# Kernel tuning notes

Hardware: AMD Instinct MI355X
Metric: run time of the kernel (lower is better)

The kernel has to match this reference:

```python
import jax, jax.numpy as jnp
import numpy as np

EMBED, HEADS, WIN, UP = 180, 6, 16, 4
HDIM = EMBED // HEADS

def _win_part(x, ws):
    # x: [B, H, W, C] -> [B*(H//ws)*(W//ws), ws, ws, C]
    B, H, W, C = x.shape
    x = x.reshape(B, H // ws, ws, W // ws, ws, C).transpose(0, 1, 3, 2, 4, 5)
    return x.reshape(-1, ws, ws, C)

def _win_rev(w, ws, H, W):
    # inverse of _win_part
    C = w.shape[-1]
    B = w.shape[0] // ((H // ws) * (W // ws))
    x = w.reshape(B, H // ws, W // ws, ws, ws, C).transpose(0, 1, 3, 2, 4, 5)
    return x.reshape(B, H, W, C)

def _ln(x, g, b):
    mu = x.mean(-1, keepdims=True)
    v = ((x - mu) ** 2).mean(-1, keepdims=True)
    return (x - mu) * jax.lax.rsqrt(v + 1e-5) * g + b

def _forward(gumbel_u, x, sel1_w, sel1_b, sel2_w, sel2_b, sel3_w, sel3_b,
             embed_w, embed_b, ln1_g, ln1_b, qkv_w, qkv_b, proj_w, proj_b,
             ln2_g, ln2_b, mlp1_w, mlp1_b, mlp2_w, mlp2_b, up_w, up_b):
    B, C, H, W = x.shape
    ws = H // 4                                     # 64 -> 16 tiles per image
    tiles = _win_part(x.transpose(0, 2, 3, 1), ws)  # [T, ws, ws, C]
    T = tiles.shape[0]
    # --- TileSelection (pooled MLP router) ---
    pooled = tiles.reshape(T, 8, ws // 8, 8, ws // 8, C).mean((2, 4)).reshape(T, 8 * 8 * C)
    f1 = pooled @ sel1_w + sel1_b
    f2 = jax.nn.relu(f1) @ sel2_w + sel2_b
    f3 = jax.nn.relu(f2) @ sel3_w + sel3_b          # [T, 2] routing logits
    # --- hard gumbel-softmax with straight-through estimator (tau=1) ---
    g = -jnp.log(-jnp.log(gumbel_u + 1e-10) + 1e-10)
    y_soft = jax.nn.softmax(f3 + g, axis=-1)
    y_hard = jax.nn.one_hot(jnp.argmax(y_soft, -1), 2, dtype=y_soft.dtype)
    pi = jax.lax.stop_gradient(y_hard - y_soft) + y_soft
    mask = pi[:, 1]                                 # 1 -> transformer expert
    # --- TR expert (SwinIR-style block, dense dispatch over all tiles) ---
    tok = tiles.reshape(T, ws * ws, C) @ embed_w + embed_b   # [T, 4096, 180]
    h = _ln(tok, ln1_g, ln1_b)
    hw = _win_part(h.reshape(T, ws, ws, EMBED), WIN).reshape(-1, WIN * WIN, EMBED)
    Nw, L = hw.shape[0], WIN * WIN
    qkv = (hw @ qkv_w + qkv_b).reshape(Nw, L, 3, HEADS, HDIM)
    q, k, v = qkv[:, :, 0], qkv[:, :, 1], qkv[:, :, 2]
    attn = jax.nn.softmax(jnp.einsum('nlhd,nmhd->nhlm', q, k) / np.sqrt(HDIM).astype(np.float32), axis=-1)
    av = jnp.einsum('nhlm,nmhd->nlhd', attn, v).reshape(Nw, L, EMBED)
    av = av @ proj_w + proj_b
    av = _win_rev(av.reshape(Nw, WIN, WIN, EMBED), WIN, ws, ws).reshape(T, ws * ws, EMBED)
    tok = tok + av
    h2 = _ln(tok, ln2_g, ln2_b)
    tok = tok + jax.nn.gelu(h2 @ mlp1_w + mlp1_b) @ mlp2_w + mlp2_b
    # pixelshuffle x4 upsample: 180 -> 3*4*4
    up = (tok @ up_w + up_b).reshape(T, ws, ws, UP, UP, C)
    up = up.transpose(0, 1, 3, 2, 4, 5).reshape(T, ws * UP, ws * UP, C)
    # --- cheap expert: bicubic x4 ---
    neg = jax.image.resize(tiles, (T, ws * UP, ws * UP, C), method='bicubic')
    # --- combine per-tile and reassemble ---
    m = mask[:, None, None, None]
    sr_tiles = m * up + (1.0 - m) * neg             # [T, 4ws, 4ws, C]
    sr = _win_rev(sr_tiles, H, H * UP, W * UP)      # [B, 4H, 4W, C]
    return sr.transpose(0, 3, 1, 2), f3, f2, f1

def setup_inputs() -> dict:
    key = jax.random.key(0)
    ks = jax.random.split(key, 16)
    B, C, H, W = 1, 3, 256, 256
    T = B * 16
    p = lambda k, s: jax.random.normal(k, s, jnp.float32) * 0.02
    return {
        'x': jax.random.normal(ks[0], (B, C, H, W), jnp.float32),
        'gumbel_u': jax.random.uniform(ks[1], (T, 2), jnp.float32),
        'sel1_w': p(ks[2], (192, 64)), 'sel1_b': jnp.zeros((64,), jnp.float32),
        'sel2_w': p(ks[3], (64, 32)), 'sel2_b': jnp.zeros((32,), jnp.float32),
        'sel3_w': p(ks[4], (32, 2)), 'sel3_b': jnp.zeros((2,), jnp.float32),
        'embed_w': p(ks[5], (3, EMBED)), 'embed_b': jnp.zeros((EMBED,), jnp.float32),
        'ln1_g': jnp.ones((EMBED,), jnp.float32), 'ln1_b': jnp.zeros((EMBED,), jnp.float32),
        'qkv_w': p(ks[6], (EMBED, 3 * EMBED)), 'qkv_b': jnp.zeros((3 * EMBED,), jnp.float32),
        'proj_w': p(ks[7], (EMBED, EMBED)), 'proj_b': jnp.zeros((EMBED,), jnp.float32),
        'ln2_g': jnp.ones((EMBED,), jnp.float32), 'ln2_b': jnp.zeros((EMBED,), jnp.float32),
        'mlp1_w': p(ks[8], (EMBED, 2 * EMBED)), 'mlp1_b': jnp.zeros((2 * EMBED,), jnp.float32),
        'mlp2_w': p(ks[9], (2 * EMBED, EMBED)), 'mlp2_b': jnp.zeros((EMBED,), jnp.float32),
        'up_w': p(ks[10], (EMBED, 3 * UP * UP)), 'up_b': jnp.zeros((3 * UP * UP,), jnp.float32),
    }

def reference(x, gumbel_u, sel1_w, sel1_b, sel2_w, sel2_b, sel3_w, sel3_b,
              embed_w, embed_b, ln1_g, ln1_b, qkv_w, qkv_b, proj_w, proj_b,
              ln2_g, ln2_b, mlp1_w, mlp1_b, mlp2_w, mlp2_b, up_w, up_b):
    return _forward(gumbel_u, x, sel1_w, sel1_b, sel2_w, sel2_b, sel3_w, sel3_b,
                    embed_w, embed_b, ln1_g, ln1_b, qkv_w, qkv_b, proj_w, proj_b,
                    ln2_g, ln2_b, mlp1_w, mlp1_b, mlp2_w, mlp2_b, up_w, up_b)
```

## Files before the change

### kernel.cpp

```cpp
#include <hip/hip_runtime.h>
#include <hip/hip_bf16.h>
#include <cstdint>

typedef __hip_bfloat16 bf16;
typedef __attribute__((ext_vector_type(8))) short short8;
typedef __attribute__((ext_vector_type(4))) short short4v;
typedef __attribute__((ext_vector_type(4))) float f32x4;
typedef __attribute__((ext_vector_type(2))) unsigned int uint2v;

__device__ __forceinline__ float bf2f(bf16 v) { return __bfloat162float(v); }
__device__ __forceinline__ bf16  f2bf(float v) { return __float2bfloat16(v); }
__device__ __forceinline__ float rbf(short s) {
  union { uint32_t u; float f; } c; c.u = ((uint32_t)(uint16_t)s) << 16; return c.f;
}
__device__ __forceinline__ short wbf(float f) {
  bf16 h = f2bf(f); return *(short*)&h;
}
__device__ __forceinline__ uint32_t pack2(float a, float b) {
  bf16 x = f2bf(a), y = f2bf(b);
  return (uint32_t)(*(uint16_t*)&x) | ((uint32_t)(*(uint16_t*)&y) << 16);
}
__device__ __forceinline__ uint2v pack4(float a, float b, float c, float d) {
  uint2v r; r[0] = pack2(a, b); r[1] = pack2(c, d); return r;
}
__device__ __forceinline__ int swz(int row, int g) { return g ^ (row & 7); }

__device__ __forceinline__ int win_to_token(int m) {
  int n = m >> 8, l = m & 255;
  int t = n >> 4, win = n & 15;
  int wi = win >> 2, wj = win & 3;
  int u = l >> 4, v = l & 15;
  return (t << 12) | ((wi * 16 + u) << 6) | (wj * 16 + v);
}

__global__ __launch_bounds__(256) void k_packsel(
    const float* __restrict__ qkvw, const float* __restrict__ projw,
    const float* __restrict__ mlp1w, const float* __restrict__ mlp2w,
    const float* __restrict__ upw, const float* __restrict__ qkvb,
    bf16* __restrict__ Bt_qkv, bf16* __restrict__ Bt_proj,
    bf16* __restrict__ Bt_mlp1, bf16* __restrict__ Bt_mlp2,
    bf16* __restrict__ Bt_up, float* __restrict__ biasq,
    const float* __restrict__ x, const float* __restrict__ gu,
    const float* __restrict__ s1w, const float* __restrict__ s1b,
    const float* __restrict__ s2w, const float* __restrict__ s2b,
    const float* __restrict__ s3w, const float* __restrict__ s3b,
    float* __restrict__ f1o, float* __restrict__ f2o, float* __restrict__ f3o,
    float* __restrict__ maskp) {
  if (blockIdx.x < 1203) {
    int idx = blockIdx.x * 256 + threadIdx.x;
    const int e0 = 576 * 192, e1 = e0 + 192 * 192, e2 = e1 + 384 * 192,
              e3 = e2 + 192 * 384, e4 = e3 + 64 * 192, e5 = e4 + 576;
    if (idx < e0) {
      int np = idx / 192, k = idx % 192;
      int buf = np / 192, colp = np % 192;
      int hd = colp >> 5, dd = colp & 31;
      float v = 0.f;
      if (dd < 30 && k < 180) v = qkvw[(size_t)k * 540 + buf * 180 + hd * 30 + dd];
      Bt_qkv[idx] = f2bf(v);
    } else if (idx < e1) {
      int off = idx - e0; int n = off / 192, kp = off % 192;
      int hd = kp >> 5, dd = kp & 31;
      float v = (dd < 30 && n < 180) ? projw[(size_t)(hd * 30 + dd) * 180 + n] : 0.f;
      Bt_proj[off] = f2bf(v);
    } else if (idx < e2) {
      int off = idx - e1; int n = off / 192, k = off % 192;
      Bt_mlp1[off] = f2bf((k < 180 && n < 360) ? mlp1w[(size_t)k * 360 + n] : 0.f);
    } else if (idx < e3) {
      int off = idx - e2; int n = off / 384, k = off % 384;
      Bt_mlp2[off] = f2bf((k < 360 && n < 180) ? mlp2w[(size_t)k * 180 + n] : 0.f);
    } else if (idx < e4) {
      int off = idx - e3; int n = off / 192, k = off % 192;
      Bt_up[off] = f2bf((k < 180 && n < 48) ? upw[(size_t)k * 48 + n] : 0.f);
    } else if (idx < e5) {
      int np = idx - e4;
      int buf = np / 192, colp = np % 192;
      int hd = colp >> 5, dd = colp & 31;
      biasq[np] = (dd < 30) ? qkvb[buf * 180 + hd * 30 + dd] : 0.f;
    }
    return;
  }
  int t = blockIdx.x - 1203;
  int tid = threadIdx.x;
  int th = t >> 2, tw = t & 3;
  __shared__ float pooled[192];
  __shared__ float red[256];
  __shared__ float f1s[64], f2s[32], f3s[2];
  if (tid < 192) {
    int ch = tid % 3, j = (tid / 3) & 7, i = tid / 24;
    const float* xp = x + ch * 65536 + (th * 64 + i * 8) * 256 + (tw * 64 + j * 8);
    float s = 0.f;
#pragma unroll
    for (int a = 0; a < 8; ++a)
#pragma unroll
      for (int b = 0; b < 8; ++b) s += xp[a * 256 + b];
    pooled[tid] = s * (1.0f / 64.0f);
  }
  __syncthreads();
  {
    int o = tid & 63, part = tid >> 6;
    float s = 0.f;
    for (int k = part * 48; k < part * 48 + 48; ++k) s = fmaf(pooled[k], s1w[k * 64 + o], s);
    red[tid] = s;
  }
  __syncthreads();
  if (tid < 64) {
    float v = red[tid] + red[tid + 64] + red[tid + 128] + red[tid + 192] + s1b[tid];
    f1o[t * 64 + tid] = v;
    f1s[tid] = fmaxf(v, 0.f);
  }
  __syncthreads();
  {
    int o = tid & 31, part = tid >> 5;
    float s = 0.f;
    for (int k = part * 8; k < part * 8 + 8; ++k) s = fmaf(f1s[k], s2w[k * 32 + o], s);
    red[tid] = s;
  }
  __syncthreads();
  if (tid < 32) {
    float v = s2b[tid];
#pragma unroll
    for (int p = 0; p < 8; ++p) v += red[tid + p * 32];
    f2o[t * 32 + tid] = v;
    f2s[tid] = fmaxf(v, 0.f);
  }
  __syncthreads();
  if (tid < 2) {
    float s = s3b[tid];
    for (int k = 0; k < 32; ++k) s = fmaf(f2s[k], s3w[k * 2 + tid], s);
    f3o[t * 2 + tid] = s;
    f3s[tid] = s;
  }
  __syncthreads();
  if (tid == 0) {
    float g0 = -logf(-logf(gu[t * 2 + 0] + 1e-10f) + 1e-10f);
    float g1 = -logf(-logf(gu[t * 2 + 1] + 1e-10f) + 1e-10f);
    maskp[t] = (f3s[1] + g1 > f3s[0] + g0) ? 1.0f : 0.0f;
  }
}

__global__ __launch_bounds__(256) void k_embed(
    const float* __restrict__ x, const float* __restrict__ ew,
    const float* __restrict__ eb, const float* __restrict__ g1,
    const float* __restrict__ b1, bf16* __restrict__ tok,
    bf16* __restrict__ Aq) {
  int wrow = blockIdx.x * 4 + (threadIdx.x >> 6);
  int lane = threadIdx.x & 63;
  int token = win_to_token(wrow);
  int t = token >> 12, p = token & 4095;
  int r = p >> 6, c = p & 63;
  int gh = (t >> 2) * 64 + r, gw = (t & 3) * 64 + c;
  float x0 = x[gh * 256 + gw];
  float x1 = x[65536 + gh * 256 + gw];
  float x2 = x[131072 + gh * 256 + gw];
  float v[3];
  float s = 0.f, s2 = 0.f;
#pragma unroll
  for (int i = 0; i < 3; ++i) {
    int e = lane + i * 64;
    float vv = 0.f;
    if (e < 180) {
      vv = eb[e];
      vv = fmaf(x0, ew[e], vv);
      vv = fmaf(x1, ew[180 + e], vv);
      vv = fmaf(x2, ew[360 + e], vv);
      tok[(size_t)wrow * 180 + e] = f2bf(vv);
      s += vv; s2 = fmaf(vv, vv, s2);
    }
    v[i] = vv;
  }
#pragma unroll
  for (int off = 32; off; off >>= 1) { s += __shfl_xor(s, off); s2 += __shfl_xor(s2, off); }
  float mu = s * (1.f / 180.f);
  float rs = rsqrtf(s2 * (1.f / 180.f) - mu * mu + 1e-5f);
#pragma unroll
  for (int i = 0; i < 3; ++i) {
    int e = lane + i * 64;
    if (e < 192) {
      float a = (e < 180) ? ((v[i] - mu) * rs * g1[e] + b1[e]) : 0.f;
      Aq[(size_t)wrow * 192 + e] = f2bf(a);
    }
  }
}

__global__ __launch_bounds__(512, 2) void k_qkv3(
    const bf16* __restrict__ A, const bf16* __restrict__ Bt,
    const float* __restrict__ biasq, bf16* __restrict__ Qp,
    bf16* __restrict__ Kp, bf16* __restrict__ Vp) {
  __shared__ bf16 Bs[2][64 * 192];
  const int tid = threadIdx.x;
  const int w = tid >> 6, l = tid & 63;
  const int lr = l & 15, lk = l >> 4;
  const int row = blockIdx.x * 128 + w * 16 + lr;

  short8 fa[6];
  {
    const bf16* Ab = A + (size_t)row * 192 + lk * 8;
#pragma unroll
    for (int ks = 0; ks < 6; ++ks) fa[ks] = *(const short8*)(Ab + ks * 32);
  }

  for (int c = tid; c < 1536; c += 512) {
    int n = c / 24, g = c % 24;
    *(short8*)&Bs[0][n * 192 + swz(n, g) * 8] = *(const short8*)(Bt + (size_t)n * 192 + g * 8);
  }

  for (int nt = 0; nt < 9; ++nt) {
    __syncthreads();
    if (nt < 8) {
      const bf16* src = Bt + (size_t)(nt + 1) * 64 * 192;
      bf16* dstb = Bs[(nt + 1) & 1];
      for (int c = tid; c < 1536; c += 512) {
        int n = c / 24, g = c % 24;
        *(short8*)&dstb[n * 192 + swz(n, g) * 8] = *(const short8*)(src + (size_t)n * 192 + g * 8);
      }
    }
    const bf16* Bb = Bs[nt & 1];
    f32x4 acc[4];
#pragma unroll
    for (int j = 0; j < 4; ++j) acc[j] = (f32x4){0.f, 0.f, 0.f, 0.f};
#pragma unroll
    for (int ks = 0; ks < 6; ++ks) {
      short8 fb[4];
#pragma unroll
      for (int j = 0; j < 4; ++j) {
        int rn = j * 16 + lr;
        fb[j] = *(const short8*)&Bb[rn * 192 + swz(rn, ks * 4 + lk) * 8];
      }
#pragma unroll
      for (int j = 0; j < 4; ++j)
        acc[j] = __builtin_amdgcn_mfma_f32_16x16x32_bf16(fb[j], fa[ks], acc[j], 0, 0, 0);
    }
    bf16* dst = (nt < 3) ? Qp : (nt < 6) ? Kp : Vp;
    int c0 = (nt % 3) * 64;
#pragma unroll
    for (int j = 0; j < 4; ++j) {
      int np = nt * 64 + j * 16 + lk * 4;
      f32x4 bv = *(const f32x4*)&biasq[np];
      *(uint2v*)(dst + (size_t)row * 192 + c0 + j * 16 + lk * 4) =
          pack4(acc[j][0] + bv[0], acc[j][1] + bv[1], acc[j][2] + bv[2], acc[j][3] + bv[3]);
    }
  }
}

__global__ __launch_bounds__(256) void k_attn2(
    const bf16* __restrict__ Qp, const bf16* __restrict__ Kp,
    const bf16* __restrict__ Vp, bf16* __restrict__ av) {
  const int blk = blockIdx.x;
  const int win = blk / 6, hd = blk % 6;
  const int tid = threadIdx.x;
  const int w = tid >> 6, l = tid & 63;
  const int lr = l & 15, lk = l >> 4;
  const float scale = 0.18257418583505536f;

  __shared__ bf16 Ks[256][40];
  __shared__ bf16 Vs[32][264];
  __shared__ bf16 Ps[4][16][264];

  {
    const bf16* src = Kp + (size_t)(win * 256 + tid) * 192 + hd * 32;
#pragma unroll
    for (int c = 0; c < 4; ++c)
      *(short8*)&Ks[tid][c * 8] = *(const short8*)(src + c * 8);
  }
  {
    const bf16* src = Vp + (size_t)(win * 256 + tid) * 192 + hd * 32;
    short8 vv[4];
#pragma unroll
    for (int c = 0; c < 4; ++c) vv[c] = *(const short8*)(src + c * 8);
#pragma unroll
    for (int c = 0; c < 4; ++c)
#pragma unroll
      for (int e = 0; e < 8; ++e)
        *(short*)&Vs[c * 8 + e][tid] = vv[c][e];
  }
  __syncthreads();

  for (int qt = 0; qt < 4; ++qt) {
    const int qbase = qt * 64 + w * 16;
    short8 fq = *(const short8*)(Qp + (size_t)(win * 256 + qbase + lr) * 192 + hd * 32 + lk * 8);
    f32x4 accS[16];
#pragma unroll
    for (int kt = 0; kt < 16; ++kt) {
      short8 fk = *(const short8*)(&Ks[kt * 16 + lr][lk * 8]);
      accS[kt] = __builtin_amdgcn_mfma_f32_16x16x32_bf16(
          fk, fq, (f32x4){0.f, 0.f, 0.f, 0.f}, 0, 0, 0);
    }
    float mraw = -1e30f;
#pragma unroll
    for (int kt = 0; kt < 16; ++kt)
#pragma unroll
      for (int r = 0; r < 4; ++r) mraw = fmaxf(mraw, accS[kt][r]);
    mraw = fmaxf(mraw, __shfl_xor(mraw, 16));
    mraw = fmaxf(mraw, __shfl_xor(mraw, 32));
    const float mc = mraw * scale;
    float lsum = 0.f;
#pragma unroll
    for (int kt = 0; kt < 16; ++kt) {
      float p0 = __expf(fmaf(accS[kt][0], scale, -mc));
      float p1 = __expf(fmaf(accS[kt][1], scale, -mc));
      float p2 = __expf(fmaf(accS[kt][2], scale, -mc));
      float p3 = __expf(fmaf(accS[kt][3], scale, -mc));
      lsum += (p0 + p1) + (p2 + p3);
      *(uint32_t*)&Ps[w][lr][kt * 16 + lk * 4]     = pack2(p0, p1);
      *(uint32_t*)&Ps[w][lr][kt * 16 + lk * 4 + 2] = pack2(p2, p3);
    }
    lsum += __shfl_xor(lsum, 16);
    lsum += __shfl_xor(lsum, 32);
    __syncthreads();
    f32x4 accO0 = (f32x4){0.f, 0.f, 0.f, 0.f};
    f32x4 accO1 = (f32x4){0.f, 0.f, 0.f, 0.f};
#pragma unroll
    for (int ks = 0; ks < 8; ++ks) {
      short8 fp  = *(const short8*)(&Ps[w][lr][ks * 32 + lk * 8]);
      short8 fv0 = *(const short8*)(&Vs[lr][ks * 32 + lk * 8]);
      short8 fv1 = *(const short8*)(&Vs[16 + lr][ks * 32 + lk * 8]);
      accO0 = __builtin_amdgcn_mfma_f32_16x16x32_bf16(fv0, fp, accO0, 0, 0, 0);
      accO1 = __builtin_amdgcn_mfma_f32_16x16x32_bf16(fv1, fp, accO1, 0, 0, 0);
    }
    float invl = 1.f / lsum;
    bf16* avrow = av + (size_t)(win * 256 + qbase + lr) * 192 + hd * 32;
    *(uint2v*)(avrow + lk * 4) =
        pack4(accO0[0] * invl, accO0[1] * invl, accO0[2] * invl, accO0[3] * invl);
    *(uint2v*)(avrow + 16 + lk * 4) =
        pack4(accO1[0] * invl, accO1[1] * invl, accO1[2] * invl, accO1[3] * invl);
    __syncthreads();
  }
}

__global__ __launch_bounds__(512, 2) void k_post(
    const bf16* __restrict__ av, const bf16* __restrict__ tok,
    const bf16* __restrict__ Btp, const float* __restrict__ pb,
    const float* __restrict__ g2, const float* __restrict__ b2,
    const bf16* __restrict__ Bt1, const float* __restrict__ b1m,
    const bf16* __restrict__ Bt2, const float* __restrict__ b2m,
    const bf16* __restrict__ Btu, const float* __restrict__ bu,
    bf16* __restrict__ up) {
  __shared__ bf16 Bs[2][64 * 192];
  __shared__ bf16 Hm[128 * 192];
  const int tid = threadIdx.x;
  const int w = tid >> 6, l = tid & 63;
  const int lr = l & 15, lk = l >> 4;
  const int row_l = w * 16 + lr;
  const int row_g = blockIdx.x * 128 + row_l;
  const int half = (lk & 1) * 4;

#define STAGE_A(srcp, dstb)                                               \
  {                                                                       \
    const bf16* _s = (srcp);                                              \
    bf16* _d = (dstb);                                                    \
    for (int c = tid; c < 1536; c += 512) {                               \
      int n = c / 24, g = c % 24;                                         \
      *(short8*)&_d[n * 192 + swz(n, g) * 8] =                            \
          *(const short8*)(_s + (size_t)n * 192 + g * 8);                 \
    }                                                                     \
  }
#define STAGE_S(ntv, dstb)                                                \
  {                                                                       \
    bf16* _d = (dstb);                                                    \
    for (int c = tid; c < 1536; c += 512) {                               \
      int n = c / 8, g = c % 8;                                           \
      *(short8*)&_d[n * 64 + swz(n, g) * 8] =                             \
          *(const short8*)(Bt2 + (size_t)n * 384 + (ntv) * 64 + g * 8);   \
    }                                                                     \
  }

  short8 fa[6];
  {
    const bf16* ab = av + (size_t)row_g * 192 + lk * 8;
#pragma unroll
    for (int ks = 0; ks < 6; ++ks) fa[ks] = *(const short8*)(ab + ks * 32);
  }

  short4v t2p[3][4];
  float sA = 0.f, s2A = 0.f;

  STAGE_A(Btp, Bs[0]);

#pragma unroll
  for (int nt = 0; nt < 3; ++nt) {
    __syncthreads();
    if (nt < 2) { STAGE_A(Btp + (size_t)(nt + 1) * 64 * 192, Bs[(nt + 1) & 1]); }
    else        { STAGE_A(Bt1, Bs[1]); }
    const bf16* Bb = Bs[nt & 1];
    f32x4 acc[4];
#pragma unroll
    for (int j = 0; j < 4; ++j) acc[j] = (f32x4){0.f, 0.f, 0.f, 0.f};
#pragma unroll
    for (int ks = 0; ks < 6; ++ks) {
      short8 fb[4];
#pragma unroll
      for (int j = 0; j < 4; ++j) {
        int rn = j * 16 + lr;
        fb[j] = *(const short8*)&Bb[rn * 192 + swz(rn, ks * 4 + lk) * 8];
      }
#pragma unroll
      for (int j = 0; j < 4; ++j)
        acc[j] = __builtin_amdgcn_mfma_f32_16x16x32_bf16(fb[j], fa[ks], acc[j], 0, 0, 0);
    }
#pragma unroll
    for (int j = 0; j < 4; ++j) {
      int n = nt * 64 + j * 16 + lk * 4;
      if (n < 180) {
        f32x4 bv = *(const f32x4*)&pb[n];
        short4v tv = *(const short4v*)(tok + (size_t)row_g * 180 + n);
#pragma unroll
        for (int q = 0; q < 4; ++q) {
          float v = acc[j][q] + bv[q] + rbf(tv[q]);
          sA += v; s2A = fmaf(v, v, s2A);
          t2p[nt][j][q] = wbf(v);
        }
      } else {
#pragma unroll
        for (int q = 0; q < 4; ++q) t2p[nt][j][q] = 0;
      }
    }
  }

  {
    sA += __shfl_xor(sA, 16);  sA += __shfl_xor(sA, 32);
    s2A += __shfl_xor(s2A, 16); s2A += __shfl_xor(s2A, 32);
    float mu = sA * (1.f / 180.f);
    float rs = rsqrtf(s2A * (1.f / 180.f) - mu * mu + 1e-5f);
#pragma unroll
    for (int nt = 0; nt < 3; ++nt)
#pragma unroll
      for (int j = 0; j < 4; ++j) {
        int n = nt * 64 + j * 16 + lk * 4;
        float h[4] = {0.f, 0.f, 0.f, 0.f};
        if (n < 180) {
          f32x4 gv = *(const f32x4*)&g2[n];
          f32x4 bv = *(const f32x4*)&b2[n];
#pragma unroll
          for (int q = 0; q < 4; ++q)
            h[q] = (rbf(t2p[nt][j][q]) - mu) * rs * gv[q] + bv[q];
        }
        int g = nt * 8 + j * 2 + (lk >> 1);
        *(uint2v*)&Hm[row_l * 192 + swz(row_l, g) * 8 + half] = pack4(h[0], h[1], h[2], h[3]);
      }
  }

  short8 fh[6];
  f32x4 acc2[3][4];
#pragma unroll
  for (int t = 0; t < 3; ++t)
#pragma unroll
    for (int j = 0; j < 4; ++j) acc2[t][j] = (f32x4){0.f, 0.f, 0.f, 0.f};

#pragma unroll
  for (int nt = 0; nt < 6; ++nt) {
    __syncthreads();
    STAGE_S(nt, Bs[0]);
    if (nt == 0) {
#pragma unroll
      for (int ks = 0; ks < 6; ++ks)
        fh[ks] = *(const short8*)&Hm[row_l * 192 + swz(row_l, ks * 4 + lk) * 8];
    }
    {
      const bf16* Bb = Bs[1];
      f32x4 acc1[4];
#pragma unroll
      for (int j = 0; j < 4; ++j) acc1[j] = (f32x4){0.f, 0.f, 0.f, 0.f};
#pragma unroll
      for (int ks = 0; ks < 6; ++ks) {
        short8 fb[4];
#pragma unroll
        for (int j = 0; j < 4; ++j) {
          int rn = j * 16 + lr;
          fb[j] = *(const short8*)&Bb[rn * 192 + swz(rn, ks * 4 + lk) * 8];
        }
#pragma unroll
        for (int j = 0; j < 4; ++j)
          acc1[j] = __builtin_amdgcn_mfma_f32_16x16x32_bf16(fb[j], fh[ks], acc1[j], 0, 0, 0);
      }
#pragma unroll
      for (int j = 0; j < 4; ++j) {
        int n = nt * 64 + j * 16 + lk * 4;
        float m4[4] = {0.f, 0.f, 0.f, 0.f};
        if (n < 360) {
          f32x4 bv = *(const f32x4*)&b1m[n];
#pragma unroll
          for (int q = 0; q < 4; ++q) {
            float v = acc1[j][q] + bv[q];
            float u = 0.7978845608028654f * (v + 0.044715f * v * v * v);
            m4[q] = v / (1.f + __expf(-2.f * u));
          }
        }
        int g = j * 2 + (lk >> 1);
        *(uint2v*)&Hm[row_l * 192 + swz(row_l, g) * 8 + half] = pack4(m4[0], m4[1], m4[2], m4[3]);
      }
    }
    __syncthreads();
    if (nt < 5) { STAGE_A(Bt1 + (size_t)(nt + 1) * 64 * 192, Bs[1]); }
    else        { STAGE_A(Btu, Bs[1]); }
    {
      short8 fm[2];
#pragma unroll
      for (int s = 0; s < 2; ++s)
        fm[s] = *(const short8*)&Hm[row_l * 192 + swz(row_l, s * 4 + lk) * 8];
#pragma unroll
      for (int s = 0; s < 2; ++s)
#pragma unroll
        for (int t = 0; t < 3; ++t)
#pragma unroll
          for (int j = 0; j < 4; ++j) {
            int rn = t * 64 + j * 16 + lr;
            short8 fb2 = *(const short8*)&Bs[0][rn * 64 + swz(rn, s * 4 + lk) * 8];
            acc2[t][j] = __builtin_amdgcn_mfma_f32_16x16x32_bf16(fb2, fm[s], acc2[t][j], 0, 0, 0);
          }
    }
  }

  __syncthreads();
#pragma unroll
  for (int t = 0; t < 3; ++t)
#pragma unroll
    for (int j = 0; j < 4; ++j) {
      int n = t * 64 + j * 16 + lk * 4;
      float o4[4] = {0.f, 0.f, 0.f, 0.f};
      if (n < 180) {
        f32x4 bv = *(const f32x4*)&b2m[n];
#pragma unroll
        for (int q = 0; q < 4; ++q) o4[q] = acc2[t][j][q] + bv[q] + rbf(t2p[t][j][q]);
      }
      int g = t * 8 + j * 2 + (lk >> 1);
      *(uint2v*)&Hm[row_l * 192 + swz(row_l, g) * 8 + half] = pack4(o4[0], o4[1], o4[2], o4[3]);
    }
  __syncthreads();

  short8 ft[6];
#pragma unroll
  for (int ks = 0; ks < 6; ++ks)
    ft[ks] = *(const short8*)&Hm[row_l * 192 + swz(row_l, ks * 4 + lk) * 8];
  f32x4 acc3[3];
#pragma unroll
  for (int j = 0; j < 3; ++j) acc3[j] = (f32x4){0.f, 0.f, 0.f, 0.f};
#pragma unroll
  for (int ks = 0; ks < 6; ++ks) {
    short8 fb[3];
#pragma unroll
    for (int j = 0; j < 3; ++j) {
      int rn = j * 16 + lr;
      fb[j] = *(const short8*)&Bs[1][rn * 192 + swz(rn, ks * 4 + lk) * 8];
    }
#pragma unroll
    for (int j = 0; j < 3; ++j)
      acc3[j] = __builtin_amdgcn_mfma_f32_16x16x32_bf16(fb[j], ft[ks], acc3[j], 0, 0, 0);
  }
#pragma unroll
  for (int j = 0; j < 3; ++j) {
    int n = j * 16 + lk * 4;
    f32x4 bv = *(const f32x4*)&bu[n];
    *(uint2v*)(up + (size_t)row_g * 48 + n) =
        pack4(acc3[j][0] + bv[0], acc3[j][1] + bv[1], acc3[j][2] + bv[2], acc3[j][3] + bv[3]);
  }
#undef STAGE_A
#undef STAGE_S
}

__device__ const float c_cubw[4][4] = {
    {-0.0439453125f, 0.3896484375f, 0.7275390625f, -0.0732421875f},
    {-0.0068359375f, 0.0908203125f, 0.9638671875f, -0.0478515625f},
    {-0.0478515625f, 0.9638671875f, 0.0908203125f, -0.0068359375f},
    {-0.0732421875f, 0.7275390625f, 0.3896484375f, -0.0439453125f},
};

__device__ __forceinline__ void cubw(int r, int ph, float* w, int& base) {
  base = r + ((ph < 2) ? -2 : -1);
  float sum = 0.f;
#pragma unroll
  for (int i = 0; i < 4; ++i) {
    int idx = base + i;
    float wi = (idx >= 0 && idx < 64) ? c_cubw[ph][i] : 0.f;
    w[i] = wi; sum += wi;
  }
  float inv = 1.f / sum;
#pragma unroll
  for (int i = 0; i < 4; ++i) w[i] *= inv;
}

__global__ __launch_bounds__(256) void k_blend(
    const bf16* __restrict__ up, const float* __restrict__ x,
    const float* __restrict__ maskp, float* __restrict__ sr) {
  int idx = blockIdx.x * 256 + threadIdx.x;
  int ch = idx >> 20;
  int rem = idx & 1048575;
  int gR = rem >> 10, gC = rem & 1023;
  int th = gR >> 8, tw = gC >> 8;
  int t = th * 4 + tw;
  int R = gR & 255, C = gC & 255;
  int r = R >> 2, a = R & 3, c = C >> 2, b = C & 3;
  float m = maskp[t];
  float outv;
  if (m > 0.5f) {
    int wi = r >> 4, u = r & 15, wj = c >> 4, v = c & 15;
    int wrow = (t * 16 + wi * 4 + wj) * 256 + u * 16 + v;
    outv = bf2f(up[(size_t)wrow * 48 + a * 12 + b * 3 + ch]);
  } else {
    float wy[4], wx[4];
    int yb, xb;
    cubw(r, a, wy, yb);
    cubw(c, b, wx, xb);
    const float* xc = x + ch * 65536;
    float neg = 0.f;
#pragma unroll
    for (int i = 0; i < 4; ++i) {
      int yi = yb + i;
      if (yi < 0 || yi > 63) continue;
      float rowsum = 0.f;
#pragma unroll
      for (int j = 0; j < 4; ++j) {
        int xj = xb + j;
        if (xj < 0 || xj > 63) continue;
        rowsum = fmaf(wx[j], xc[(th * 64 + yi) * 256 + tw * 64 + xj], rowsum);
      }
      neg = fmaf(wy[i], rowsum, neg);
    }
    outv = neg;
  }
  sr[idx] = outv;
}

extern "C" void kernel_launch(void* const* d_in, const int* in_sizes, int n_in,
                              void* d_out, int out_size, void* d_ws, size_t ws_size,
                              hipStream_t stream) {
  const float* x     = (const float*)d_in[0];
  const float* gu    = (const float*)d_in[1];
  const float* s1w   = (const float*)d_in[2];
  const float* s1b   = (const float*)d_in[3];
  const float* s2w   = (const float*)d_in[4];
  const float* s2b   = (const float*)d_in[5];
  const float* s3w   = (const float*)d_in[6];
  const float* s3b   = (const float*)d_in[7];
  const float* ew    = (const float*)d_in[8];
  const float* ebias = (const float*)d_in[9];
  const float* ln1g  = (const float*)d_in[10];
  const float* ln1b  = (const float*)d_in[11];
  const float* qkvw  = (const float*)d_in[12];
  const float* qkvb  = (const float*)d_in[13];
  const float* projw = (const float*)d_in[14];
  const float* projb = (const float*)d_in[15];
  const float* ln2g  = (const float*)d_in[16];
  const float* ln2b  = (const float*)d_in[17];
  const float* mlp1w = (const float*)d_in[18];
  const float* mlp1b = (const float*)d_in[19];
  const float* mlp2w = (const float*)d_in[20];
  const float* mlp2b = (const float*)d_in[21];
  const float* upw   = (const float*)d_in[22];
  const float* upb   = (const float*)d_in[23];

  float* out = (float*)d_out;
  float* sr  = out;
  float* f3o = out + 3145728;
  float* f2o = f3o + 32;
  float* f1o = f2o + 512;

  char* ws = (char*)d_ws;
  bf16* tok  = (bf16*)(ws);
  bf16* ABuf = (bf16*)(ws + 23592960);
  bf16* Qp   = (bf16*)(ws + 48758784);
  bf16* Kp   = (bf16*)(ws + 73924608);
  bf16* Vp   = (bf16*)(ws + 99090432);
  float* maskp   = (float*)(ws + 124256256);
  bf16* Bt_qkv  = (bf16*)(ws + 124256320);
  bf16* Bt_proj = (bf16*)(ws + 124477504);
  bf16* Bt_mlp1 = (bf16*)(ws + 124551232);
  bf16* Bt_mlp2 = (bf16*)(ws + 124698688);
  bf16* Bt_up   = (bf16*)(ws + 124846144);
  float* biasq  = (float*)(ws + 124870720);
  bf16* up      = (bf16*)(ws + 124873088);
  bf16* av = ABuf;

  k_packsel<<<1219, 256, 0, stream>>>(qkvw, projw, mlp1w, mlp2w, upw, qkvb,
                                      Bt_qkv, Bt_proj, Bt_mlp1, Bt_mlp2, Bt_up, biasq,
                                      x, gu, s1w, s1b, s2w, s2b, s3w, s3b,
                                      f1o, f2o, f3o, maskp);
  k_embed<<<16384, 256, 0, stream>>>(x, ew, ebias, ln1g, ln1b, tok, ABuf);
  k_qkv3<<<512, 512, 0, stream>>>(ABuf, Bt_qkv, biasq, Qp, Kp, Vp);
  k_attn2<<<1536, 256, 0, stream>>>(Qp, Kp, Vp, av);
  k_post<<<512, 512, 0, stream>>>(av, tok, Bt_proj, projb, ln2g, ln2b,
                                  Bt_mlp1, mlp1b, Bt_mlp2, mlp2b, Bt_up, upb, up);
  k_blend<<<12288, 256, 0, stream>>>(up, x, maskp, sr);
}
```

Before: 203.9 us.

## Replace LDS round-trip with cross-lane shuffles in k_post and shrink shared buffer

The k_post kernel no longer writes the LayerNorm output and the MLP residual output to a 128x192 LDS tile and reads them back as MFMA B-fragments. It packs them in registers and rebuilds the operand layout with __shfl gathers, so the staging tile shrinks to a 128x64 buffer used only for the MLP hidden chunk. Less LDS per block, plus launch bounds raised from 2 to 4 blocks per CU, are meant to raise occupancy and drop a barrier. The cost is more shuffle instructions and tighter register limits, which may cause spills.

```diff
diff --git a/kernel.cpp b/kernel.cpp
--- a/kernel.cpp
+++ b/kernel.cpp
@@ -327,7 +327,7 @@
   }
 }
 
-__global__ __launch_bounds__(512, 2) void k_post(
+__global__ __launch_bounds__(512, 4) void k_post(
     const bf16* __restrict__ av, const bf16* __restrict__ tok,
     const bf16* __restrict__ Btp, const float* __restrict__ pb,
     const float* __restrict__ g2, const float* __restrict__ b2,
@@ -336,13 +336,16 @@
     const bf16* __restrict__ Btu, const float* __restrict__ bu,
     bf16* __restrict__ up) {
   __shared__ bf16 Bs[2][64 * 192];
-  __shared__ bf16 Hm[128 * 192];
+  __shared__ bf16 Hmid[128 * 64];
   const int tid = threadIdx.x;
   const int w = tid >> 6, l = tid & 63;
   const int lr = l & 15, lk = l >> 4;
   const int row_l = w * 16 + lr;
   const int row_g = blockIdx.x * 128 + row_l;
   const int half = (lk & 1) * 4;
+  const int sa = lr + 32 * (lk & 1);
+  const int sb = sa + 16;
+  const bool hi2 = (lk >= 2);
 
 #define STAGE_A(srcp, dstb)                                               \
   {                                                                       \
@@ -363,6 +366,24 @@
           *(const short8*)(Bt2 + (size_t)n * 384 + (ntv) * 64 + g * 8);   \
     }                                                                     \
   }
+#define GATHER_FH(dstf, pk, ksv)                                          \
+  {                                                                       \
+    const int _nt = (ksv) >> 1, _jA = ((ksv) & 1) * 2, _jB = _jA + 1;     \
+    uint32_t _a0 = (uint32_t)__shfl((int)pk[_nt][_jA][0], sa);            \
+    uint32_t _a1 = (uint32_t)__shfl((int)pk[_nt][_jA][1], sa);            \
+    uint32_t _b0 = (uint32_t)__shfl((int)pk[_nt][_jB][0], sa);            \
+    uint32_t _b1 = (uint32_t)__shfl((int)pk[_nt][_jB][1], sa);            \
+    uint32_t _c0 = (uint32_t)__shfl((int)pk[_nt][_jA][0], sb);            \
+    uint32_t _c1 = (uint32_t)__shfl((int)pk[_nt][_jA][1], sb);            \
+    uint32_t _d0 = (uint32_t)__shfl((int)pk[_nt][_jB][0], sb);            \
+    uint32_t _d1 = (uint32_t)__shfl((int)pk[_nt][_jB][1], sb);            \
+    uint32_t _t[4];                                                       \
+    _t[0] = hi2 ? _b0 : _a0;                                              \
+    _t[1] = hi2 ? _b1 : _a1;                                              \
+    _t[2] = hi2 ? _d0 : _c0;                                              \
+    _t[3] = hi2 ? _d1 : _c1;                                              \
+    __builtin_memcpy(&(dstf), _t, 16);                                    \
+  }
 
   short8 fa[6];
   {
@@ -416,11 +437,13 @@
     }
   }
 
+  short8 fh[6];
   {
     sA += __shfl_xor(sA, 16);  sA += __shfl_xor(sA, 32);
     s2A += __shfl_xor(s2A, 16); s2A += __shfl_xor(s2A, 32);
     float mu = sA * (1.f / 180.f);
     float rs = rsqrtf(s2A * (1.f / 180.f) - mu * mu + 1e-5f);
+    uint2v hpk[3][4];
 #pragma unroll
     for (int nt = 0; nt < 3; ++nt)
 #pragma unroll
@@ -434,12 +457,12 @@
           for (int q = 0; q < 4; ++q)
             h[q] = (rbf(t2p[nt][j][q]) - mu) * rs * gv[q] + bv[q];
         }
-        int g = nt * 8 + j * 2 + (lk >> 1);
-        *(uint2v*)&Hm[row_l * 192 + swz(row_l, g) * 8 + half] = pack4(h[0], h[1], h[2], h[3]);
-      }
-  }
-
-  short8 fh[6];
+        hpk[nt][j] = pack4(h[0], h[1], h[2], h[3]);
+      }
+#pragma unroll
+    for (int ks = 0; ks < 6; ++ks) GATHER_FH(fh[ks], hpk, ks);
+  }
+
   f32x4 acc2[3][4];
 #pragma unroll
   for (int t = 0; t < 3; ++t)
@@ -450,11 +473,6 @@
   for (int nt = 0; nt < 6; ++nt) {
     __syncthreads();
     STAGE_S(nt, Bs[0]);
-    if (nt == 0) {
-#pragma unroll
-      for (int ks = 0; ks < 6; ++ks)
-        fh[ks] = *(const short8*)&Hm[row_l * 192 + swz(row_l, ks * 4 + lk) * 8];
-    }
     {
       const bf16* Bb = Bs[1];
       f32x4 acc1[4];
@@ -486,7 +504,7 @@
           }
         }
         int g = j * 2 + (lk >> 1);
-        *(uint2v*)&Hm[row_l * 192 + swz(row_l, g) * 8 + half] = pack4(m4[0], m4[1], m4[2], m4[3]);
+        *(uint2v*)&Hmid[row_l * 64 + swz(row_l, g) * 8 + half] = pack4(m4[0], m4[1], m4[2], m4[3]);
       }
     }
     __syncthreads();
@@ -496,7 +514,7 @@
       short8 fm[2];
 #pragma unroll
       for (int s = 0; s < 2; ++s)
-        fm[s] = *(const short8*)&Hm[row_l * 192 + swz(row_l, s * 4 + lk) * 8];
+        fm[s] = *(const short8*)&Hmid[row_l * 64 + swz(row_l, s * 4 + lk) * 8];
 #pragma unroll
       for (int s = 0; s < 2; ++s)
 #pragma unroll
@@ -511,26 +529,26 @@
   }
 
   __syncthreads();
-#pragma unroll
-  for (int t = 0; t < 3; ++t)
-#pragma unroll
-    for (int j = 0; j < 4; ++j) {
-      int n = t * 64 + j * 16 + lk * 4;
-      float o4[4] = {0.f, 0.f, 0.f, 0.f};
-      if (n < 180) {
-        f32x4 bv = *(const f32x4*)&b2m[n];
-#pragma unroll
-        for (int q = 0; q < 4; ++q) o4[q] = acc2[t][j][q] + bv[q] + rbf(t2p[t][j][q]);
-      }
-      int g = t * 8 + j * 2 + (lk >> 1);
-      *(uint2v*)&Hm[row_l * 192 + swz(row_l, g) * 8 + half] = pack4(o4[0], o4[1], o4[2], o4[3]);
-    }
-  __syncthreads();
-
   short8 ft[6];
-#pragma unroll
-  for (int ks = 0; ks < 6; ++ks)
-    ft[ks] = *(const short8*)&Hm[row_l * 192 + swz(row_l, ks * 4 + lk) * 8];
+  {
+    uint2v tpk[3][4];
+#pragma unroll
+    for (int t = 0; t < 3; ++t)
+#pragma unroll
+      for (int j = 0; j < 4; ++j) {
+        int n = t * 64 + j * 16 + lk * 4;
+        float o4[4] = {0.f, 0.f, 0.f, 0.f};
+        if (n < 180) {
+          f32x4 bv = *(const f32x4*)&b2m[n];
+#pragma unroll
+          for (int q = 0; q < 4; ++q) o4[q] = acc2[t][j][q] + bv[q] + rbf(t2p[t][j][q]);
+        }
+        tpk[t][j] = pack4(o4[0], o4[1], o4[2], o4[3]);
+      }
+#pragma unroll
+    for (int ks = 0; ks < 6; ++ks) GATHER_FH(ft[ks], tpk, ks);
+  }
+
   f32x4 acc3[3];
 #pragma unroll
   for (int j = 0; j < 3; ++j) acc3[j] = (f32x4){0.f, 0.f, 0.f, 0.f};
@@ -555,6 +573,7 @@
   }
 #undef STAGE_A
 #undef STAGE_S
+#undef GATHER_FH
 }
 
 __device__ const float c_cubw[4][4] = {
```

After: 214.9 us. 5.4% more time.
